# Kernel optimization log

Measured on AMD Instinct MI355X. Metric: run time of the kernel, lower is better.

The kernel has to match this reference:

```python
import jax, jax.numpy as jnp
import numpy as np

B, RES, NS, W, S = 2, 64, 24, 256, 256
IN_VIEW = W + 3


def setup_inputs() -> dict:
    key = jax.random.key(0)
    ks = iter(jax.random.split(key, 32))
    u = lambda k, shape, a: jax.random.uniform(k, shape, jnp.float32, -a, a)
    c_hid = float(np.sqrt(6.0 / W) / 25.0)      # SIREN hidden init bound
    c_view = float(np.sqrt(6.0 / IN_VIEW) / 25.0)
    inp = {}
    # camera: identity rotation, camera at z=1 looking down -z (StyleSDF-like)
    pose = np.zeros((B, 3, 4), np.float32)
    pose[:, 0, 0] = 1.0; pose[:, 1, 1] = 1.0; pose[:, 2, 2] = 1.0; pose[:, 2, 3] = 1.0
    inp['cam_poses'] = jnp.asarray(pose)
    inp['focal'] = jnp.full((B, 1, 1), 87.0, jnp.float32)
    inp['near'] = jnp.full((B, 1, 1), 0.88, jnp.float32)
    inp['far'] = jnp.full((B, 1, 1), 1.12, jnp.float32)
    inp['styles'] = jax.random.normal(next(ks), (B, S), jnp.float32)
    # FiLM-SIREN point layers
    inp['w0'] = u(next(ks), (W, 3), 1.0 / 3.0)
    inp['b0'] = u(next(ks), (W,), float(np.sqrt(1.0 / 3.0)))
    inp['ws'] = u(next(ks), (7, W, W), c_hid)
    inp['bs'] = u(next(ks), (7, W), float(np.sqrt(1.0 / W)))
    inp['gamma_w'] = 0.02 * jax.random.normal(next(ks), (8, W, S), jnp.float32)
    inp['gamma_b'] = u(next(ks), (8, W), float(np.sqrt(1.0 / S)))
    inp['beta_w'] = 0.02 * jax.random.normal(next(ks), (8, W, S), jnp.float32)
    inp['beta_b'] = u(next(ks), (8, W), float(np.sqrt(1.0 / S)))
    # view-conditioned FiLM layer
    inp['view_w'] = u(next(ks), (W, IN_VIEW), c_view)
    inp['view_b'] = u(next(ks), (W,), float(np.sqrt(1.0 / IN_VIEW)))
    inp['view_gw'] = 0.02 * jax.random.normal(next(ks), (W, S), jnp.float32)
    inp['view_gb'] = u(next(ks), (W,), float(np.sqrt(1.0 / S)))
    inp['view_bw'] = 0.02 * jax.random.normal(next(ks), (W, S), jnp.float32)
    inp['view_bb'] = u(next(ks), (W,), float(np.sqrt(1.0 / S)))
    # output heads (freq_init)
    inp['rgb_w'] = u(next(ks), (3, W), c_hid)
    inp['rgb_b'] = u(next(ks), (3,), float(np.sqrt(1.0 / W)))
    inp['sigma_w'] = u(next(ks), (1, W), c_hid)
    inp['sigma_b'] = u(next(ks), (1,), float(np.sqrt(1.0 / W)))
    inp['sigmoid_beta'] = 0.1 * jnp.ones((1,), jnp.float32)
    return inp


def _film(x, style, w, b, gw, gb, bw, bb):
    # x: [B,h,w,n,in] ; FiLM-SIREN: sin(gamma * (xW^T + b) + beta)
    out = jnp.einsum('bhwni,oi->bhwno', x, w) + b
    gamma = 15.0 * (style @ gw.T + gb) + 30.0          # LinearLayer(std=15, bias_init=30)
    beta = 0.25 * (style @ bw.T + bb)                  # LinearLayer(std=0.25, bias_init=0)
    return jnp.sin(gamma[:, None, None, None, :] * out + beta[:, None, None, None, :])


def _forward(cam_poses, focal, near, far, styles, w0, b0, ws, bs, gamma_w, gamma_b,
             beta_w, beta_b, view_w, view_b, view_gw, view_gb, view_bw, view_bb,
             rgb_w, rgb_b, sigma_w, sigma_b, sigmoid_beta):
    b = cam_poses.shape[0]
    # --- get_rays (buffers i, j from meshgrid, transposed) ---
    lin = jnp.linspace(0.5, RES - 0.5, RES)
    ii = jnp.broadcast_to(lin[None, :], (RES, RES))[None]  # varies along width
    jj = jnp.broadcast_to(lin[:, None], (RES, RES))[None]  # varies along height
    dirs = jnp.stack([
        jnp.broadcast_to((ii - RES * 0.5) / focal, (b, RES, RES)),
        jnp.broadcast_to(-(jj - RES * 0.5) / focal, (b, RES, RES)),
        -jnp.ones((b, RES, RES), focal.dtype)], -1)        # [B,h,w,3]
    rays_d = jnp.einsum('bhwc,bkc->bhwk', dirs, cam_poses[:, :3, :3])
    rays_o = jnp.broadcast_to(cam_poses[:, None, None, :3, -1], rays_d.shape)
    viewdirs = rays_d / jnp.linalg.norm(rays_d, axis=-1, keepdims=True)
    # --- render_rays (test: perturb=0) ---
    near4 = near[..., None] * jnp.ones_like(rays_d[..., :1])   # [B,h,w,1]
    far4 = far[..., None] * jnp.ones_like(rays_d[..., :1])
    t_vals = jnp.linspace(0.0, 1.0 - 1.0 / NS, NS)             # offset_sampling
    z_vals = near4 * (1.0 - t_vals) + far4 * t_vals            # [B,h,w,NS]
    pts = rays_o[..., None, :] + rays_d[..., None, :] * z_vals[..., None]  # [B,h,w,NS,3]
    norm_pts = pts * (2.0 / (far4 - near4))[..., None, :]      # z_normalize
    # --- SirenGenerator (styles.ndim==2 path, no hyper deltas) ---
    h = _film(norm_pts, styles, w0, b0, gamma_w[0], gamma_b[0], beta_w[0], beta_b[0])
    for i in range(7):
        h = _film(h, styles, ws[i], bs[i], gamma_w[i + 1], gamma_b[i + 1],
                  beta_w[i + 1], beta_b[i + 1])
    sdf = jnp.einsum('bhwni,oi->bhwno', h, sigma_w) + sigma_b  # [B,h,w,NS,1]
    dirs_exp = jnp.broadcast_to(viewdirs[..., None, :], pts.shape)
    h = jnp.concatenate([h, dirs_exp], -1)                     # [B,h,w,NS,W+3]
    feat = _film(h, styles, view_w, view_b, view_gw, view_gb, view_bw, view_bb)
    rgb = jnp.einsum('bhwni,oi->bhwno', feat, rgb_w) + rgb_b   # [B,h,w,NS,3]
    # --- volume_integration (with_sdf, test: no noise) ---
    rays_d_norm = jnp.linalg.norm(rays_d, axis=-1, keepdims=True)        # [B,h,w,1]
    dists = jnp.concatenate([z_vals[..., 1:] - z_vals[..., :-1],
                             jnp.full_like(rays_d_norm, 1e10)], -1)      # [B,h,w,NS]
    dists = dists * rays_d_norm
    sigma = jax.nn.sigmoid(-sdf / sigmoid_beta) / sigmoid_beta
    alpha = 1.0 - jnp.exp(-sigma * dists[..., None])                      # [B,h,w,NS,1]
    ones = jnp.ones_like(alpha[..., :1, :])
    vis = jnp.cumprod(jnp.concatenate([ones, 1.0 - alpha + 1e-10], 3), 3)[..., :-1, :]
    weights = alpha * vis
    # force_background: last sample absorbs the remaining transmittance
    bg = 1.0 - jnp.sum(weights[..., :-1, :], axis=3)
    weights = jnp.concatenate([weights[..., :-1, :], bg[..., None, :]], 3)
    rgb_map = -1.0 + 2.0 * jnp.sum(weights * jax.nn.sigmoid(rgb), axis=3)  # [B,h,w,3]
    feature_map = jnp.sum(weights * feat, axis=3)                          # [B,h,w,W]
    return jnp.concatenate([rgb_map, feature_map], -1)                     # [B,h,w,3+W]


def reference(cam_poses, focal, near, far, styles, w0, b0, ws, bs, gamma_w, gamma_b,
              beta_w, beta_b, view_w, view_b, view_gw, view_gb, view_bw, view_bb,
              rgb_w, rgb_b, sigma_w, sigma_b, sigmoid_beta):
    return _forward(cam_poses, focal, near, far, styles, w0, b0, ws, bs, gamma_w,
                    gamma_b, beta_w, beta_b, view_w, view_b, view_gw, view_gb,
                    view_bw, view_bb, rgb_w, rgb_b, sigma_w, sigma_b, sigmoid_beta)
```

## Files before the change

kernel.cpp:

```cpp
#include <hip/hip_runtime.h>
#include <hip/hip_bf16.h>

#define RESN 64
#define NS 24
#define WD 256
#define SD 256
#define NB 2
#define RPB 4
#define MP 96
#define NTH 512
#define NBLK 2048

typedef unsigned short u16;
typedef unsigned int u32;
typedef __attribute__((ext_vector_type(8))) short short8v;
typedef __attribute__((ext_vector_type(16))) float f32x16;

__device__ __forceinline__ float sigm(float x){ return 1.0f / (1.0f + expf(-x)); }

__device__ __forceinline__ float fast_sin(float x){
  float k = __builtin_rintf(x * 0.31830988618f);
  float y = fmaf(k, -3.14159274101f, x);
  y = fmaf(k, 8.74227766e-8f, y);
  float y2 = y * y;
  float p = fmaf(y2, 2.75573192e-6f, -1.98412698e-4f);
  p = fmaf(y2, p, 8.33333333e-3f);
  p = fmaf(y2, p, -1.66666667e-1f);
  float s = fmaf(y * y2, p, y);
  u32 sg = ((u32)((int)k) & 1u) << 31;
  return __uint_as_float(__float_as_uint(s) ^ sg);
}

__global__ void prep_kernel(const float* wsp, const float* vw, u16* Whi, u16* Wlo){
  int i0 = (blockIdx.x * 256 + threadIdx.x) * 4;
  #pragma unroll
  for (int j = 0; j < 4; j++){
    int e = i0 + j;
    int lay = e >> 16;
    int rk = e & 65535;
    float w = (lay < 7) ? wsp[lay * 65536 + rk]
                        : vw[(size_t)(rk >> 8) * 259 + (rk & 255)];
    u32 b = __float_as_uint(w);
    u16 hi = (u16)(b >> 16);
    float lof = w - __uint_as_float(b & 0xFFFF0000u);
    Whi[e] = hi;
    Wlo[e] = (u16)(__float_as_uint(lof) >> 16);
  }
}

__global__ void film_kernel(const float* styles, const float* gw8, const float* gb8,
                            const float* bw8, const float* bb8,
                            const float* vgw, const float* vgb, const float* vbw, const float* vbb,
                            float* G, float* Bt){
  int l = blockIdx.x >> 1, b = blockIdx.x & 1, o = threadIdx.x;
  __shared__ float st[SD];
  st[o] = styles[b * SD + o];
  __syncthreads();
  const float *gw, *bw; float gbv, bbv;
  if (l < 8){
    gw = gw8 + ((size_t)l * WD + o) * SD; bw = bw8 + ((size_t)l * WD + o) * SD;
    gbv = gb8[l * WD + o];                bbv = bb8[l * WD + o];
  } else {
    gw = vgw + (size_t)o * SD;            bw = vbw + (size_t)o * SD;
    gbv = vgb[o];                         bbv = vbb[o];
  }
  float ag = 0.f, ab = 0.f;
  for (int s = 0; s < SD; s += 2){
    ag += st[s] * gw[s] + st[s+1] * gw[s+1];
    ab += st[s] * bw[s] + st[s+1] * bw[s+1];
  }
  int idx = (l * NB + b) * WD + o;
  G[idx]  = 15.0f * (ag + gbv) + 30.0f;
  Bt[idx] = 0.25f * (ab + bbv);
}

#define SETW(LAY) { wph = Whi + (((size_t)(LAY) * WD + col) * WD) + khalf * 8;   \
                    wpl = Wlo + (((size_t)(LAY) * WD + col) * WD) + khalf * 8; }

#define PREF4 { _Pragma("unroll")                                                \
  for (int i = 0; i < 4; i++){                                                   \
    pbh[i] = *(const short8v*)(wph + i * 16);                                    \
    pbl[i] = *(const short8v*)(wpl + i * 16); } }

#define KMAIN                                                                    \
  _Pragma("unroll")                                                              \
  for (int ks = 0; ks < 16; ks++){                                               \
    short8v bh = pbh[ks & 3], bl = pbl[ks & 3];                                  \
    if (ks < 12){ pbh[ks & 3] = *(const short8v*)(wph + (ks + 4) * 16);          \
                  pbl[ks & 3] = *(const short8v*)(wpl + (ks + 4) * 16); }        \
    int ce = 2 * ks + khalf;                                                     \
    _Pragma("unroll")                                                            \
    for (int mt = 0; mt < 3; mt++){                                              \
      int elem = (mt * 32 + lane31) * WD + ((ce ^ l7) * 8);                      \
      short8v ah = *(const short8v*)(&Hhi[elem]);                                \
      short8v al = *(const short8v*)(&Hlo[elem]);                                \
      acc[mt] = __builtin_amdgcn_mfma_f32_32x32x16_bf16(bh, ah, acc[mt], 0,0,0); \
      acc[mt] = __builtin_amdgcn_mfma_f32_32x32x16_bf16(bh, al, acc[mt], 0,0,0); \
      acc[mt] = __builtin_amdgcn_mfma_f32_32x32x16_bf16(bl, ah, acc[mt], 0,0,0); \
    } }

__launch_bounds__(NTH, 2)
__global__ void render_mfma(
    const float* pose, const float* focal, const float* nearv, const float* farv,
    const float* w0, const float* b0, const float* bsp,
    const float* vw, const float* vb,
    const float* rgbw, const float* rgbb, const float* sgw, const float* sgb,
    const float* sbeta, const float* G, const float* Bt,
    const u16* Whi, const u16* Wlo, float* out)
{
  __shared__ u16 Hhi[MP * WD];
  __shared__ u16 Hlo[MP * WD];
  __shared__ float xl[MP][4];
  __shared__ float vd[RPB][4];
  __shared__ float dn[RPB];
  __shared__ float sdfl[MP];
  __shared__ float rgbl[MP][4];
  __shared__ float wtl[RPB][NS];
  __shared__ float swl[WD];
  __shared__ float rwl[3][WD];

  const int t      = threadIdx.x;
  const int lane   = t & 63;
  const int wv     = t >> 6;
  const int lane31 = lane & 31;
  const int khalf  = lane >> 5;
  const int l7     = lane31 & 7;
  const int col    = wv * 32 + lane31;
  const int om     = t & 127;
  const int mg     = t >> 7;
  const int o0     = om * 2, o1 = om * 2 + 1;
  const int mb     = mg * NS;
  const int ray0   = blockIdx.x * RPB;
  const int bidx   = ray0 >> 12;

  const u16 *wph, *wpl;
  short8v pbh[4], pbl[4];
  SETW(0); PREF4;

  if (t < WD) swl[t] = sgw[t];
  for (int i = t; i < 3 * WD; i += NTH) ((float*)rwl)[i] = rgbw[i];

  if (t < MP){
    int m = t, s = m % NS, rl = m / NS;
    int ray = ray0 + rl;
    int ww = ray & (RESN - 1);
    int hh = (ray >> 6) & (RESN - 1);
    float f = focal[bidx], nr = nearv[bidx], fr = farv[bidx];
    float di = ((ww + 0.5f) - RESN * 0.5f) / f;
    float dj = -(((hh + 0.5f) - RESN * 0.5f) / f);
    const float* P = pose + bidx * 12;
    float rdx = di * P[0] + dj * P[1] - P[2];
    float rdy = di * P[4] + dj * P[5] - P[6];
    float rdz = di * P[8] + dj * P[9] - P[10];
    float ox = P[3], oy = P[7], oz = P[11];
    float nrm = sqrtf(rdx * rdx + rdy * rdy + rdz * rdz);
    const float C = (1.0f - 1.0f / NS) / (NS - 1);
    float tv = s * C;
    float z = nr * (1.0f - tv) + fr * tv;
    float sc = 2.0f / (fr - nr);
    xl[m][0] = (ox + rdx * z) * sc;
    xl[m][1] = (oy + rdy * z) * sc;
    xl[m][2] = (oz + rdz * z) * sc;
    if (s == 0){
      vd[rl][0] = rdx / nrm; vd[rl][1] = rdy / nrm; vd[rl][2] = rdz / nrm;
      dn[rl] = nrm;
    }
  }
  __syncthreads();

  {
    float wa[3], wbv[3];
    #pragma unroll
    for (int j = 0; j < 3; j++){ wa[j] = w0[o0 * 3 + j]; wbv[j] = w0[o1 * 3 + j]; }
    float bi0 = b0[o0], bi1 = b0[o1];
    float g0 = G[bidx * WD + o0],  g1 = G[bidx * WD + o1];
    float e0 = Bt[bidx * WD + o0], e1 = Bt[bidx * WD + o1];
    #pragma unroll
    for (int m = 0; m < NS; m++){
      int row = mb + m;
      float x0 = xl[row][0], x1 = xl[row][1], x2 = xl[row][2];
      float u0 = x0 * wa[0]  + x1 * wa[1]  + x2 * wa[2]  + bi0;
      float u1 = x0 * wbv[0] + x1 * wbv[1] + x2 * wbv[2] + bi1;
      float s0 = fast_sin(fmaf(g0, u0, e0));
      float s1 = fast_sin(fmaf(g1, u1, e1));
      u32 bs0 = __float_as_uint(s0), bs1 = __float_as_uint(s1);
      u32 hw = (bs0 >> 16) | (bs1 & 0xFFFF0000u);
      float l0f = s0 - __uint_as_float(bs0 & 0xFFFF0000u);
      float l1f = s1 - __uint_as_float(bs1 & 0xFFFF0000u);
      u32 lw = (__float_as_uint(l0f) >> 16) | (__float_as_uint(l1f) & 0xFFFF0000u);
      int eidx = row * WD + (((o0 >> 3) ^ (row & 7)) * 8) + (o0 & 7);
      *(u32*)&Hhi[eidx] = hw;
      *(u32*)&Hlo[eidx] = lw;
    }
  }
  __syncthreads();

  #pragma unroll 1
  for (int l = 0; l < 7; l++){
    f32x16 acc[3];
    #pragma unroll
    for (int mt = 0; mt < 3; mt++)
      #pragma unroll
      for (int j = 0; j < 16; j++) acc[mt][j] = 0.f;
    KMAIN
    int gi = (l + 1) * NB + bidx;
    __syncthreads();
    #pragma unroll
    for (int q = 0; q < 4; q++){
      int cq = wv * 32 + q * 8 + khalf * 4;
      float4 g4 = *(const float4*)&G[gi * WD + cq];
      float4 e4 = *(const float4*)&Bt[gi * WD + cq];
      float4 b4 = *(const float4*)&bsp[l * WD + cq];
      int slotc = (wv * 4 + q);
      #pragma unroll
      for (int mt = 0; mt < 3; mt++){
        int row = mt * 32 + lane31;
        u32 hp[4], lp[4];
        #pragma unroll
        for (int i = 0; i < 4; i++){
          float a = acc[mt][q * 4 + i] + b4[i];
          float s = fast_sin(fmaf(g4[i], a, e4[i]));
          u32 sb = __float_as_uint(s);
          hp[i] = sb >> 16;
          float sl = s - __uint_as_float(sb & 0xFFFF0000u);
          lp[i] = __float_as_uint(sl) >> 16;
        }
        int idx = row * WD + ((slotc ^ (row & 7)) * 8) + khalf * 4;
        uint2 H; H.x = hp[0] | (hp[1] << 16); H.y = hp[2] | (hp[3] << 16);
        uint2 L; L.x = lp[0] | (lp[1] << 16); L.y = lp[2] | (lp[3] << 16);
        *(uint2*)&Hhi[idx] = H;
        *(uint2*)&Hlo[idx] = L;
      }
    }
    SETW(l + 1); PREF4;
    __syncthreads();
  }

  f32x16 acc[3];
  #pragma unroll
  for (int mt = 0; mt < 3; mt++)
    #pragma unroll
    for (int j = 0; j < 16; j++) acc[mt][j] = 0.f;
  KMAIN

  if (t < MP){
    float a = 0.f;
    #pragma unroll 4
    for (int c = 0; c < 32; c++){
      int eb = t * WD + ((c ^ (t & 7)) * 8);
      short8v hv = *(const short8v*)(&Hhi[eb]);
      short8v lv = *(const short8v*)(&Hlo[eb]);
      #pragma unroll
      for (int j = 0; j < 8; j++){
        float h = __uint_as_float(((u32)(u16)hv[j]) << 16)
                + __uint_as_float(((u32)(u16)lv[j]) << 16);
        a = fmaf(h, swl[c * 8 + j], a);
      }
    }
    sdfl[t] = a + sgb[0];
  }
  __syncthreads();

  {
    int gi8 = (8 * NB + bidx) * WD;
    #pragma unroll
    for (int q = 0; q < 4; q++){
      int cq = wv * 32 + q * 8 + khalf * 4;
      float t0q[4], t1q[4], t2q[4];
      #pragma unroll
      for (int i = 0; i < 4; i++){
        const float* vr = vw + (size_t)(cq + i) * 259;
        t0q[i] = vr[256]; t1q[i] = vr[257]; t2q[i] = vr[258];
      }
      float4 vb4 = *(const float4*)&vb[cq];
      float4 g4  = *(const float4*)&G[gi8 + cq];
      float4 e4  = *(const float4*)&Bt[gi8 + cq];
      int slotc = (wv * 4 + q);
      #pragma unroll
      for (int mt = 0; mt < 3; mt++){
        int row = mt * 32 + lane31;
        int rayi = (row >= 48) ? ((row >= 72) ? 3 : 2) : ((row >= 24) ? 1 : 0);
        float d0 = vd[rayi][0], d1 = vd[rayi][1], d2 = vd[rayi][2];
        u32 hp[4], lp[4];
        #pragma unroll
        for (int i = 0; i < 4; i++){
          float c = d0 * t0q[i] + d1 * t1q[i] + d2 * t2q[i] + vb4[i];
          float a = acc[mt][q * 4 + i] + c;
          float s = fast_sin(fmaf(g4[i], a, e4[i]));
          u32 sb = __float_as_uint(s);
          hp[i] = sb >> 16;
          float sl = s - __uint_as_float(sb & 0xFFFF0000u);
          lp[i] = __float_as_uint(sl) >> 16;
        }
        int idx = row * WD + ((slotc ^ (row & 7)) * 8) + khalf * 4;
        uint2 H; H.x = hp[0] | (hp[1] << 16); H.y = hp[2] | (hp[3] << 16);
        uint2 L; L.x = lp[0] | (lp[1] << 16); L.y = lp[2] | (lp[3] << 16);
        *(uint2*)&Hhi[idx] = H;
        *(uint2*)&Hlo[idx] = L;
      }
    }
  }
  __syncthreads();

  if (t < MP){
    float a0 = 0.f, a1 = 0.f, a2 = 0.f;
    #pragma unroll 4
    for (int c = 0; c < 32; c++){
      int eb = t * WD + ((c ^ (t & 7)) * 8);
      short8v hv = *(const short8v*)(&Hhi[eb]);
      short8v lv = *(const short8v*)(&Hlo[eb]);
      #pragma unroll
      for (int j = 0; j < 8; j++){
        float h = __uint_as_float(((u32)(u16)hv[j]) << 16)
                + __uint_as_float(((u32)(u16)lv[j]) << 16);
        int k = c * 8 + j;
        a0 = fmaf(h, rwl[0][k], a0);
        a1 = fmaf(h, rwl[1][k], a1);
        a2 = fmaf(h, rwl[2][k], a2);
      }
    }
    rgbl[t][0] = a0 + rgbb[0];
    rgbl[t][1] = a1 + rgbb[1];
    rgbl[t][2] = a2 + rgbb[2];
  }
  __syncthreads();

  if (t < RPB){
    int r = t;
    int ray = ray0 + r;
    float nr = nearv[bidx], fr = farv[bidx];
    float dnv = dn[r];
    float bet = sbeta[0];
    float vis = 1.f, wsum = 0.f, cr = 0.f, cg = 0.f, cb = 0.f;
    const float C = (1.0f - 1.0f / NS) / (NS - 1);
    #pragma unroll
    for (int s = 0; s < NS; s++){
      float w;
      if (s < NS - 1){
        float t0v = s * C, t1v = (s + 1) * C;
        float z0 = nr * (1.f - t0v) + fr * t0v;
        float z1 = nr * (1.f - t1v) + fr * t1v;
        float dist = (z1 - z0) * dnv;
        float sg = sigm(-sdfl[r * NS + s] / bet) / bet;
        float al = 1.f - expf(-sg * dist);
        w = al * vis;
        vis *= (1.f - al + 1e-10f);
        wsum += w;
      } else {
        w = 1.f - wsum;
      }
      wtl[r][s] = w;
      cr += w * sigm(rgbl[r * NS + s][0]);
      cg += w * sigm(rgbl[r * NS + s][1]);
      cb += w * sigm(rgbl[r * NS + s][2]);
    }
    size_t ob = (size_t)ray * 259;
    out[ob + 0] = -1.f + 2.f * cr;
    out[ob + 1] = -1.f + 2.f * cg;
    out[ob + 2] = -1.f + 2.f * cb;
  }
  __syncthreads();

  {
    float f0 = 0.f, f1 = 0.f;
    #pragma unroll
    for (int s = 0; s < NS; s++){
      int row = mb + s;
      float w = wtl[mg][s];
      int eidx = row * WD + (((o0 >> 3) ^ (row & 7)) * 8) + (o0 & 7);
      u32 wh = *(const u32*)&Hhi[eidx];
      u32 wl = *(const u32*)&Hlo[eidx];
      float fa = __uint_as_float(wh << 16) + __uint_as_float(wl << 16);
      float fb = __uint_as_float(wh & 0xFFFF0000u) + __uint_as_float(wl & 0xFFFF0000u);
      f0 = fmaf(w, fa, f0);
      f1 = fmaf(w, fb, f1);
    }
    size_t ob = (size_t)(ray0 + mg) * 259 + 3;
    out[ob + o0] = f0;
    out[ob + o1] = f1;
  }
}

extern "C" void kernel_launch(void* const* d_in, const int* in_sizes, int n_in,
                              void* d_out, int out_size, void* d_ws, size_t ws_size,
                              hipStream_t stream) {
  (void)in_sizes; (void)n_in; (void)out_size; (void)ws_size;
  const float* pose   = (const float*)d_in[0];
  const float* focal  = (const float*)d_in[1];
  const float* nearv  = (const float*)d_in[2];
  const float* farv   = (const float*)d_in[3];
  const float* styles = (const float*)d_in[4];
  const float* w0     = (const float*)d_in[5];
  const float* b0     = (const float*)d_in[6];
  const float* wsp    = (const float*)d_in[7];
  const float* bsp    = (const float*)d_in[8];
  const float* gw8    = (const float*)d_in[9];
  const float* gb8    = (const float*)d_in[10];
  const float* bw8    = (const float*)d_in[11];
  const float* bb8    = (const float*)d_in[12];
  const float* vw     = (const float*)d_in[13];
  const float* vb     = (const float*)d_in[14];
  const float* vgw    = (const float*)d_in[15];
  const float* vgb    = (const float*)d_in[16];
  const float* vbw    = (const float*)d_in[17];
  const float* vbb    = (const float*)d_in[18];
  const float* rgbw   = (const float*)d_in[19];
  const float* rgbb   = (const float*)d_in[20];
  const float* sgw    = (const float*)d_in[21];
  const float* sgb    = (const float*)d_in[22];
  const float* sbeta  = (const float*)d_in[23];

  float* G  = (float*)d_ws;
  float* Bt = G + 9 * NB * WD;
  float* out = (float*)d_out;

  const size_t plane_off = 36864;
  const size_t plane_elems = (size_t)8 * WD * WD;

  u16* Whi = (u16*)((char*)d_ws + plane_off);
  u16* Wlo = Whi + plane_elems;

  film_kernel<<<dim3(18), dim3(256), 0, stream>>>(styles, gw8, gb8, bw8, bb8,
                                                  vgw, vgb, vbw, vbb, G, Bt);
  prep_kernel<<<dim3(512), dim3(256), 0, stream>>>(wsp, vw, Whi, Wlo);
  render_mfma<<<dim3(NBLK), dim3(NTH), 0, stream>>>(pose, focal, nearv, farv,
      w0, b0, bsp, vw, vb, rgbw, rgbb, sgw, sgb, sbeta, G, Bt, Whi, Wlo, out);
}
```

Measured before the change: 869.8 us.

## Software-pipeline MFMA layers by interleaving sine epilogue with the next tile's matmul

```diff
diff --git a/kernel.cpp b/kernel.cpp
--- a/kernel.cpp
+++ b/kernel.cpp
@@ -82,22 +82,70 @@
     pbh[i] = *(const short8v*)(wph + i * 16);                                    \
     pbl[i] = *(const short8v*)(wpl + i * 16); } }
 
-#define KMAIN                                                                    \
+#define EPIH(J, AC, MT, Q) {                                                     \
+  int gi_ = ((J) + 1) * NB + bidx;                                               \
+  int cq_ = wv * 32 + (Q) * 8 + khalf * 4;                                       \
+  float4 g4_ = *(const float4*)&G[gi_ * WD + cq_];                               \
+  float4 e4_ = *(const float4*)&Bt[gi_ * WD + cq_];                              \
+  float4 b4_ = *(const float4*)&bsp[(J) * WD + cq_];                             \
+  int slotc_ = wv * 4 + (Q);                                                     \
+  int row_ = (MT) * 32 + lane31;                                                 \
+  u32 hp_[4], lp_[4];                                                            \
+  _Pragma("unroll")                                                              \
+  for (int i_ = 0; i_ < 4; i_++){                                                \
+    float a_ = AC[(Q) * 4 + i_] + b4_[i_];                                       \
+    float s_ = fast_sin(fmaf(g4_[i_], a_, e4_[i_]));                             \
+    u32 sb_ = __float_as_uint(s_);                                               \
+    hp_[i_] = sb_ >> 16;                                                         \
+    float sl_ = s_ - __uint_as_float(sb_ & 0xFFFF0000u);                         \
+    lp_[i_] = __float_as_uint(sl_) >> 16;                                        \
+  }                                                                              \
+  int idx_ = row_ * WD + ((slotc_ ^ (row_ & 7)) * 8) + khalf * 4;                \
+  uint2 H_; H_.x = hp_[0] | (hp_[1] << 16); H_.y = hp_[2] | (hp_[3] << 16);      \
+  uint2 L_; L_.x = lp_[0] | (lp_[1] << 16); L_.y = lp_[2] | (lp_[3] << 16);      \
+  *(uint2*)&Hhi[idx_] = H_;                                                      \
+  *(uint2*)&Hlo[idx_] = L_; }
+
+#define KSA(DOEPI, EPJ)                                                          \
   _Pragma("unroll")                                                              \
   for (int ks = 0; ks < 16; ks++){                                               \
     short8v bh = pbh[ks & 3], bl = pbl[ks & 3];                                  \
     if (ks < 12){ pbh[ks & 3] = *(const short8v*)(wph + (ks + 4) * 16);          \
                   pbl[ks & 3] = *(const short8v*)(wpl + (ks + 4) * 16); }        \
     int ce = 2 * ks + khalf;                                                     \
-    _Pragma("unroll")                                                            \
-    for (int mt = 0; mt < 3; mt++){                                              \
-      int elem = (mt * 32 + lane31) * WD + ((ce ^ l7) * 8);                      \
-      short8v ah = *(const short8v*)(&Hhi[elem]);                                \
-      short8v al = *(const short8v*)(&Hlo[elem]);                                \
-      acc[mt] = __builtin_amdgcn_mfma_f32_32x32x16_bf16(bh, ah, acc[mt], 0,0,0); \
-      acc[mt] = __builtin_amdgcn_mfma_f32_32x32x16_bf16(bh, al, acc[mt], 0,0,0); \
-      acc[mt] = __builtin_amdgcn_mfma_f32_32x32x16_bf16(bl, ah, acc[mt], 0,0,0); \
-    } }
+    { int e_ = (lane31) * WD + ((ce ^ l7) * 8);                                  \
+      short8v ah = *(const short8v*)(&Hhi[e_]);                                  \
+      short8v al = *(const short8v*)(&Hlo[e_]);                                  \
+      acc0 = __builtin_amdgcn_mfma_f32_32x32x16_bf16(bh, ah, acc0, 0,0,0);       \
+      acc0 = __builtin_amdgcn_mfma_f32_32x32x16_bf16(bh, al, acc0, 0,0,0);       \
+      acc0 = __builtin_amdgcn_mfma_f32_32x32x16_bf16(bl, ah, acc0, 0,0,0); }     \
+    { int e_ = (32 + lane31) * WD + ((ce ^ l7) * 8);                             \
+      short8v ah = *(const short8v*)(&Hhi[e_]);                                  \
+      short8v al = *(const short8v*)(&Hlo[e_]);                                  \
+      acc1 = __builtin_amdgcn_mfma_f32_32x32x16_bf16(bh, ah, acc1, 0,0,0);       \
+      acc1 = __builtin_amdgcn_mfma_f32_32x32x16_bf16(bh, al, acc1, 0,0,0);       \
+      acc1 = __builtin_amdgcn_mfma_f32_32x32x16_bf16(bl, ah, acc1, 0,0,0); }     \
+    if ((DOEPI) && (ks & 3) == 3){ EPIH(EPJ, acc2, 2, (ks >> 2)) }               \
+  }
+
+#define KSB(EPJ)                                                                 \
+  _Pragma("unroll")                                                              \
+  for (int ks = 0; ks < 16; ks++){                                               \
+    short8v bh = pbh[ks & 3], bl = pbl[ks & 3];                                  \
+    if (ks < 12){ pbh[ks & 3] = *(const short8v*)(wph + (ks + 4) * 16);          \
+                  pbl[ks & 3] = *(const short8v*)(wpl + (ks + 4) * 16); }        \
+    int ce = 2 * ks + khalf;                                                     \
+    { int e_ = (64 + lane31) * WD + ((ce ^ l7) * 8);                             \
+      short8v ah = *(const short8v*)(&Hhi[e_]);                                  \
+      short8v al = *(const short8v*)(&Hlo[e_]);                                  \
+      acc2 = __builtin_amdgcn_mfma_f32_32x32x16_bf16(bh, ah, acc2, 0,0,0);       \
+      acc2 = __builtin_amdgcn_mfma_f32_32x32x16_bf16(bh, al, acc2, 0,0,0);       \
+      acc2 = __builtin_amdgcn_mfma_f32_32x32x16_bf16(bl, ah, acc2, 0,0,0); }     \
+    if (ks & 1){ int q8 = ks >> 1;                                               \
+      if (q8 < 4){ EPIH(EPJ, acc0, 0, q8) } else { EPIH(EPJ, acc1, 1, (q8 - 4)) } } \
+  }
+
+#define ZACC(A) { _Pragma("unroll") for (int j_ = 0; j_ < 16; j_++) A[j_] = 0.f; }
 
 __launch_bounds__(NTH, 2)
 __global__ void render_mfma(
@@ -136,6 +184,8 @@
   const u16 *wph, *wpl;
   short8v pbh[4], pbl[4];
   SETW(0); PREF4;
+
+  f32x16 acc0, acc1, acc2;
 
   if (t < WD) swl[t] = sgw[t];
   for (int i = t; i < 3 * WD; i += NTH) ((float*)rwl)[i] = rgbw[i];
@@ -197,52 +247,37 @@
 
   #pragma unroll 1
   for (int l = 0; l < 7; l++){
-    f32x16 acc[3];
-    #pragma unroll
-    for (int mt = 0; mt < 3; mt++)
-      #pragma unroll
-      for (int j = 0; j < 16; j++) acc[mt][j] = 0.f;
-    KMAIN
-    int gi = (l + 1) * NB + bidx;
+    ZACC(acc0) ZACC(acc1)
+    if (l > 0){ KSA(1, (l - 1)) } else { KSA(0, 0) }
+    SETW(l); PREF4;
     __syncthreads();
-    #pragma unroll
-    for (int q = 0; q < 4; q++){
-      int cq = wv * 32 + q * 8 + khalf * 4;
-      float4 g4 = *(const float4*)&G[gi * WD + cq];
-      float4 e4 = *(const float4*)&Bt[gi * WD + cq];
-      float4 b4 = *(const float4*)&bsp[l * WD + cq];
-      int slotc = (wv * 4 + q);
-      #pragma unroll
-      for (int mt = 0; mt < 3; mt++){
-        int row = mt * 32 + lane31;
-        u32 hp[4], lp[4];
-        #pragma unroll
-        for (int i = 0; i < 4; i++){
-          float a = acc[mt][q * 4 + i] + b4[i];
-          float s = fast_sin(fmaf(g4[i], a, e4[i]));
-          u32 sb = __float_as_uint(s);
-          hp[i] = sb >> 16;
-          float sl = s - __uint_as_float(sb & 0xFFFF0000u);
-          lp[i] = __float_as_uint(sl) >> 16;
-        }
-        int idx = row * WD + ((slotc ^ (row & 7)) * 8) + khalf * 4;
-        uint2 H; H.x = hp[0] | (hp[1] << 16); H.y = hp[2] | (hp[3] << 16);
-        uint2 L; L.x = lp[0] | (lp[1] << 16); L.y = lp[2] | (lp[3] << 16);
-        *(uint2*)&Hhi[idx] = H;
-        *(uint2*)&Hlo[idx] = L;
-      }
-    }
+    ZACC(acc2)
+    KSB(l)
     SETW(l + 1); PREF4;
     __syncthreads();
   }
 
-  f32x16 acc[3];
-  #pragma unroll
-  for (int mt = 0; mt < 3; mt++)
-    #pragma unroll
-    for (int j = 0; j < 16; j++) acc[mt][j] = 0.f;
-  KMAIN
-
+  ZACC(acc0) ZACC(acc1)
+  KSA(1, 6)
+  SETW(7); PREF4;
+  __syncthreads();
+
+  ZACC(acc2)
+  {
+    _Pragma("unroll")
+    for (int ks = 0; ks < 16; ks++){
+      short8v bh = pbh[ks & 3], bl = pbl[ks & 3];
+      if (ks < 12){ pbh[ks & 3] = *(const short8v*)(wph + (ks + 4) * 16);
+                    pbl[ks & 3] = *(const short8v*)(wpl + (ks + 4) * 16); }
+      int ce = 2 * ks + khalf;
+      int e_ = (64 + lane31) * WD + ((ce ^ l7) * 8);
+      short8v ah = *(const short8v*)(&Hhi[e_]);
+      short8v al = *(const short8v*)(&Hlo[e_]);
+      acc2 = __builtin_amdgcn_mfma_f32_32x32x16_bf16(bh, ah, acc2, 0,0,0);
+      acc2 = __builtin_amdgcn_mfma_f32_32x32x16_bf16(bh, al, acc2, 0,0,0);
+      acc2 = __builtin_amdgcn_mfma_f32_32x32x16_bf16(bl, ah, acc2, 0,0,0);
+    }
+  }
   if (t < MP){
     float a = 0.f;
     #pragma unroll 4
@@ -285,7 +320,8 @@
         #pragma unroll
         for (int i = 0; i < 4; i++){
           float c = d0 * t0q[i] + d1 * t1q[i] + d2 * t2q[i] + vb4[i];
-          float a = acc[mt][q * 4 + i] + c;
+          float a = ((mt == 0) ? acc0[q * 4 + i] : (mt == 1) ? acc1[q * 4 + i]
+                                                            : acc2[q * 4 + i]) + c;
           float s = fast_sin(fmaf(g4[i], a, e4[i]));
           u32 sb = __float_as_uint(s);
           hp[i] = sb >> 16;
```

New measurement: 1.276 ms. 46.7% more time.
